# Performance work log

Measured on AMD Instinct MI355X. Metric: run time of the kernel, lower is better.

## Reference

```python
import itertools
import jax, jax.numpy as jnp
import numpy as np

N = 8  # entities per sample; 8! = 40320 permutations -> exact assignment by enumeration
_PERMS = np.array(list(itertools.permutations(range(N))), dtype=np.int32)  # [P, N]


def setup_inputs() -> dict:
    key = jax.random.key(0)
    k1, k2 = jax.random.split(key)
    B, D = 2048, 64
    y_true = jax.random.normal(k1, (B, N, D), dtype=jnp.float32)
    y_pred = jax.random.normal(k2, (B, N, D), dtype=jnp.float32)
    return {"y_true": y_true, "y_pred": y_pred}


def reference(y_true, y_pred):
    # Pairwise cost matrix: C[b, i, j] = mean_d (y_true[b,i,d] - y_pred[b,j,d])^2
    diff = y_true[:, :, None, :] - y_pred[:, None, :, :]   # [B, N, N, D]
    C = jnp.mean(jnp.square(diff), axis=-1)                 # [B, N, N]

    # Exact Hungarian matching: minimize sum_i C[i, pi(i)] over permutations pi.
    # N is small, so enumerate all N! permutations (identical optimum to
    # scipy.optimize.linear_sum_assignment used in the original tf.py_function).
    perms = jnp.asarray(_PERMS)                             # [P, N]
    rows = jnp.arange(N)[None, :]                           # [1, N]
    matched = C[:, rows, perms]                             # [B, P, N] gathered costs
    totals = matched.sum(axis=-1)                           # [B, P]
    best = jnp.min(totals, axis=-1) / N                     # [B] mean matched cost
    return jnp.mean(best)                                   # scalar loss
```

## Files before the change

### kernel.cpp

```cpp
#include <hip/hip_runtime.h>

#define WAVES_PER_BLOCK 4
#define NBATCH 2048
#define NROWS 8
#define NDIM 64
#define ROW_PITCH 68
#define NBLOCKS (NBATCH / WAVES_PER_BLOCK)

__global__ __launch_bounds__(WAVES_PER_BLOCK * 64)
void assignment_stage1(const float* __restrict__ y_true,
                       const float* __restrict__ y_pred,
                       float* __restrict__ partials) {
    __shared__ float s_yt[WAVES_PER_BLOCK][NROWS * ROW_PITCH];
    __shared__ float s_yp[WAVES_PER_BLOCK][NROWS * ROW_PITCH];
    __shared__ float s_C [WAVES_PER_BLOCK][64];
    __shared__ float s_dp[WAVES_PER_BLOCK][256];
    __shared__ float s_wsum[WAVES_PER_BLOCK];

    const int lane = threadIdx.x & 63;
    const int wv   = threadIdx.x >> 6;
    const int b    = blockIdx.x * WAVES_PER_BLOCK + wv;

    const float* tb = y_true + (size_t)b * (NROWS * NDIM);
    const float* pb = y_pred + (size_t)b * (NROWS * NDIM);

    #pragma unroll
    for (int k = 0; k < 2; ++k) {
        int l   = 4 * lane + 256 * k;
        int row = l >> 6;
        int d   = l & 63;
        float4 vt = *(const float4*)(tb + l);
        float4 vp = *(const float4*)(pb + l);
        *(float4*)&s_yt[wv][row * ROW_PITCH + d] = vt;
        *(float4*)&s_yp[wv][row * ROW_PITCH + d] = vp;
    }
    __syncthreads();

    {
        const int i = lane >> 3;
        const int j = lane & 7;
        const float* ai = &s_yt[wv][i * ROW_PITCH];
        const float* pj = &s_yp[wv][j * ROW_PITCH];
        float a0 = 0.f, a1 = 0.f, a2 = 0.f, a3 = 0.f;
        #pragma unroll
        for (int d = 0; d < NDIM; d += 4) {
            float4 va = *(const float4*)(ai + d);
            float4 vp = *(const float4*)(pj + d);
            float d0 = va.x - vp.x, d1 = va.y - vp.y;
            float d2 = va.z - vp.z, d3 = va.w - vp.w;
            a0 = fmaf(d0, d0, a0); a1 = fmaf(d1, d1, a1);
            a2 = fmaf(d2, d2, a2); a3 = fmaf(d3, d3, a3);
        }
        s_C[wv][lane] = (a0 + a1) + (a2 + a3);
    }
    if (lane == 0) s_dp[wv][0] = 0.0f;
    __syncthreads();

    #pragma unroll
    for (int lv = 1; lv <= 8; ++lv) {
        const int r8 = (lv - 1) * 8;
        #pragma unroll
        for (int q = 0; q < 4; ++q) {
            int m = q * 64 + lane;
            if (__popc(m) == lv) {
                float best = 1e30f;
                #pragma unroll
                for (int j = 0; j < 8; ++j) {
                    if (m & (1 << j)) {
                        float v = s_dp[wv][m ^ (1 << j)] + s_C[wv][r8 + j];
                        best = fminf(best, v);
                    }
                }
                s_dp[wv][m] = best;
            }
        }
        __syncthreads();
    }

    if (lane == 0) s_wsum[wv] = s_dp[wv][255];
    __syncthreads();
    if (threadIdx.x == 0)
        partials[blockIdx.x] = (s_wsum[0] + s_wsum[1]) + (s_wsum[2] + s_wsum[3]);
}

__global__ __launch_bounds__(256)
void assignment_stage2(const float* __restrict__ partials,
                       float* __restrict__ out) {
    __shared__ float s[WAVES_PER_BLOCK];
    const int t = threadIdx.x;
    float v = partials[t] + partials[t + 256];
    #pragma unroll
    for (int off = 32; off > 0; off >>= 1)
        v += __shfl_down(v, off, 64);
    if ((t & 63) == 0) s[t >> 6] = v;
    __syncthreads();
    if (t == 0)
        out[0] = ((s[0] + s[1]) + (s[2] + s[3])) * (1.0f / (64.0f * 8.0f * 2048.0f));
}

extern "C" void kernel_launch(void* const* d_in, const int* in_sizes, int n_in,
                              void* d_out, int out_size, void* d_ws, size_t ws_size,
                              hipStream_t stream) {
    const float* y_true = (const float*)d_in[0];
    const float* y_pred = (const float*)d_in[1];
    float* partials = (float*)d_ws;
    float* out = (float*)d_out;

    assignment_stage1<<<NBLOCKS, WAVES_PER_BLOCK * 64, 0, stream>>>(y_true, y_pred, partials);
    assignment_stage2<<<1, 256, 0, stream>>>(partials, out);
}
```

Measured before the change: 69.64 us.

## Run subset DP in registers with wave shuffles, one wave per sample

Moves the bitmask DP over row subsets out of shared memory into registers. Each lane holds four DP entries, and predecessor states are read through cross-lane shuffle-xor for the low six bits and register swaps for the top two. The cost matrix is broadcast by shuffles, so block-wide __syncthreads between DP levels are gone. Blocks shrink to one wave per sample and stage2 now reduces 2048 partials; the trade is more shuffle and ALU work per level, since every lane computes all candidates and masks them.

```diff
diff --git a/kernel.cpp b/kernel.cpp
--- a/kernel.cpp
+++ b/kernel.cpp
@@ -1,26 +1,19 @@
 #include <hip/hip_runtime.h>
 
-#define WAVES_PER_BLOCK 4
 #define NBATCH 2048
 #define NROWS 8
 #define NDIM 64
 #define ROW_PITCH 68
-#define NBLOCKS (NBATCH / WAVES_PER_BLOCK)
 
-__global__ __launch_bounds__(WAVES_PER_BLOCK * 64)
+__global__ __launch_bounds__(64)
 void assignment_stage1(const float* __restrict__ y_true,
                        const float* __restrict__ y_pred,
                        float* __restrict__ partials) {
-    __shared__ float s_yt[WAVES_PER_BLOCK][NROWS * ROW_PITCH];
-    __shared__ float s_yp[WAVES_PER_BLOCK][NROWS * ROW_PITCH];
-    __shared__ float s_C [WAVES_PER_BLOCK][64];
-    __shared__ float s_dp[WAVES_PER_BLOCK][256];
-    __shared__ float s_wsum[WAVES_PER_BLOCK];
+    __shared__ float s_yt[NROWS * ROW_PITCH];
+    __shared__ float s_yp[NROWS * ROW_PITCH];
 
-    const int lane = threadIdx.x & 63;
-    const int wv   = threadIdx.x >> 6;
-    const int b    = blockIdx.x * WAVES_PER_BLOCK + wv;
-
+    const int lane = threadIdx.x;
+    const int b    = blockIdx.x;
     const float* tb = y_true + (size_t)b * (NROWS * NDIM);
     const float* pb = y_pred + (size_t)b * (NROWS * NDIM);
 
@@ -29,18 +22,17 @@
         int l   = 4 * lane + 256 * k;
         int row = l >> 6;
         int d   = l & 63;
-        float4 vt = *(const float4*)(tb + l);
-        float4 vp = *(const float4*)(pb + l);
-        *(float4*)&s_yt[wv][row * ROW_PITCH + d] = vt;
-        *(float4*)&s_yp[wv][row * ROW_PITCH + d] = vp;
+        *(float4*)&s_yt[row * ROW_PITCH + d] = *(const float4*)(tb + l);
+        *(float4*)&s_yp[row * ROW_PITCH + d] = *(const float4*)(pb + l);
     }
     __syncthreads();
 
+    float myC;
     {
         const int i = lane >> 3;
         const int j = lane & 7;
-        const float* ai = &s_yt[wv][i * ROW_PITCH];
-        const float* pj = &s_yp[wv][j * ROW_PITCH];
+        const float* ai = &s_yt[i * ROW_PITCH];
+        const float* pj = &s_yp[j * ROW_PITCH];
         float a0 = 0.f, a1 = 0.f, a2 = 0.f, a3 = 0.f;
         #pragma unroll
         for (int d = 0; d < NDIM; d += 4) {
@@ -51,44 +43,55 @@
             a0 = fmaf(d0, d0, a0); a1 = fmaf(d1, d1, a1);
             a2 = fmaf(d2, d2, a2); a3 = fmaf(d3, d3, a3);
         }
-        s_C[wv][lane] = (a0 + a1) + (a2 + a3);
+        myC = (a0 + a1) + (a2 + a3);
     }
-    if (lane == 0) s_dp[wv][0] = 0.0f;
-    __syncthreads();
+
+    const float INF = 1e30f;
+    float dp[4];
+    dp[0] = (lane == 0) ? 0.f : INF;
+    dp[1] = INF; dp[2] = INF; dp[3] = INF;
 
     #pragma unroll
     for (int lv = 1; lv <= 8; ++lv) {
         const int r8 = (lv - 1) * 8;
+        float c[8];
+        #pragma unroll
+        for (int j = 0; j < 8; ++j)
+            c[j] = __shfl(myC, r8 + j, 64);
+
+        float nd[4];
         #pragma unroll
         for (int q = 0; q < 4; ++q) {
-            int m = q * 64 + lane;
-            if (__popc(m) == lv) {
-                float best = 1e30f;
-                #pragma unroll
-                for (int j = 0; j < 8; ++j) {
-                    if (m & (1 << j)) {
-                        float v = s_dp[wv][m ^ (1 << j)] + s_C[wv][r8 + j];
-                        best = fminf(best, v);
-                    }
-                }
-                s_dp[wv][m] = best;
+            const int m = q * 64 + lane;
+            float best = INF;
+            #pragma unroll
+            for (int j = 0; j < 6; ++j) {
+                float v = __shfl_xor(dp[q], 1 << j, 64) + c[j];
+                best = ((m >> j) & 1) ? fminf(best, v) : best;
             }
+            if (q & 1) best = fminf(best, dp[q ^ 1] + c[6]);
+            if (q & 2) best = fminf(best, dp[q ^ 2] + c[7]);
+            nd[q] = best;
         }
-        __syncthreads();
+        #pragma unroll
+        for (int q = 0; q < 4; ++q) {
+            const int m = q * 64 + lane;
+            dp[q] = (__popc(m) == lv) ? nd[q] : dp[q];
+        }
     }
 
-    if (lane == 0) s_wsum[wv] = s_dp[wv][255];
-    __syncthreads();
-    if (threadIdx.x == 0)
-        partials[blockIdx.x] = (s_wsum[0] + s_wsum[1]) + (s_wsum[2] + s_wsum[3]);
+    float r = __shfl(dp[3], 63, 64);
+    if (lane == 0) partials[b] = r;
 }
 
 __global__ __launch_bounds__(256)
 void assignment_stage2(const float* __restrict__ partials,
                        float* __restrict__ out) {
-    __shared__ float s[WAVES_PER_BLOCK];
+    __shared__ float s[4];
     const int t = threadIdx.x;
-    float v = partials[t] + partials[t + 256];
+    float v = 0.f;
+    #pragma unroll
+    for (int k = 0; k < 8; ++k) v += partials[t + 256 * k];
     #pragma unroll
     for (int off = 32; off > 0; off >>= 1)
         v += __shfl_down(v, off, 64);
@@ -106,6 +109,6 @@
     float* partials = (float*)d_ws;
     float* out = (float*)d_out;
 
-    assignment_stage1<<<NBLOCKS, WAVES_PER_BLOCK * 64, 0, stream>>>(y_true, y_pred, partials);
+    assignment_stage1<<<NBATCH, 64, 0, stream>>>(y_true, y_pred, partials);
     assignment_stage2<<<1, 256, 0, stream>>>(partials, out);
 }
```

Result: faster. 65.38 us (-6.1%).
